# Kernel tuning notes

Hardware: AMD Instinct MI355X
Metric: run time of the kernel (lower is better)

The kernel has to match this reference:

```python
import jax, jax.numpy as jnp
import numpy as np

B, N, D = 2, 8192, 1024
H, DH = 8, 64  # heads, dim_head; inner = H*DH = 512
INNER = H * DH


def setup_inputs() -> dict:
    key = jax.random.key(0)
    k1, k2, k3 = jax.random.split(key, 3)
    x = jax.random.normal(k1, (B, N, D), dtype=jnp.float32)
    # xavier_uniform-ish scaling for weights
    W_qkv = jax.random.normal(k2, (D, 3 * INNER), dtype=jnp.float32) * (1.0 / np.sqrt(D))
    W_out = jax.random.normal(k3, (INNER, D), dtype=jnp.float32) * (1.0 / np.sqrt(INNER))
    b_out = jnp.zeros((D,), dtype=jnp.float32)
    return {"x": x, "W_qkv": W_qkv, "W_out": W_out, "b_out": b_out}


def reference(x, W_qkv, W_out, b_out):
    b, n, d = x.shape
    qkv = x @ W_qkv                               # [b, n, 3*inner]
    q, k, v = jnp.split(qkv, 3, axis=-1)          # each [b, n, inner]

    def to_heads(t):
        return t.reshape(b, n, H, DH).transpose(0, 2, 1, 3)  # [b, h, n, dh]

    q, k, v = to_heads(q), to_heads(k), to_heads(v)
    q = jax.nn.softmax(q, axis=-1)                # over dim_head
    k = jax.nn.softmax(k, axis=-2)                # over sequence
    # context: k^T v  -> [b, h, dh, dh]
    context = jnp.einsum('bhnd,bhne->bhde', k, v)
    out = jnp.einsum('bhnd,bhde->bhne', q, context)  # [b, h, n, dh]
    out = out.transpose(0, 2, 1, 3).reshape(b, n, INNER)
    return out @ W_out + b_out                    # [b, n, d]
```

## Files before the change

kernel.cpp:

```cpp
#include <hip/hip_runtime.h>
#include <stdint.h>


typedef _Float16 half4 __attribute__((ext_vector_type(4)));
typedef _Float16 half8 __attribute__((ext_vector_type(8)));
typedef float f32x4 __attribute__((ext_vector_type(4)));

#define WS_XB 0UL
#define WS_WQKVT 33554432UL
#define WS_CWT 37748736UL
#define WS_EKH 54525952UL
#define WS_VH 71303168UL
#define WS_SQ 88080384UL
#define WS_CTXPART 104857600UL
#define WS_COLPART 113246208UL
#define WS_CTX 113377280UL

__device__ __forceinline__ void gld16(const void* g, void* l) {
  __builtin_amdgcn_global_load_lds(
      (const __attribute__((address_space(1))) unsigned int*)g,
      (__attribute__((address_space(3))) unsigned int*)l, 16, 0, 0);
}

__global__ void prep_kernel(const float* __restrict__ x,
                            const float* __restrict__ Wqkv,
                            _Float16* __restrict__ xb,
                            _Float16* __restrict__ wqkvT) {
  const int blk = blockIdx.x;
  if (blk < 16384) {
    int i = blk * 256 + threadIdx.x;
    f32x4 v = *(const f32x4*)(x + (size_t)i * 4);
    half4 h = {(_Float16)v[0], (_Float16)v[1], (_Float16)v[2], (_Float16)v[3]};
    *(half4*)(xb + (size_t)i * 4) = h;
  } else {
    int i = (blk - 16384) * 256 + threadIdx.x;
    int c = i >> 10, r = i & 1023;
    wqkvT[i] = (_Float16)Wqkv[(size_t)r * 1536 + c];
  }
}


__device__ __forceinline__ void stage_tile(const _Float16* __restrict__ G, int K,
                                           int rowbase, int kt, char* region,
                                           int t) {
  char* wbase = region + (t & ~63) * 16;
#pragma unroll
  for (int q = 0; q < 4; ++q) {
    const int row = q * 32 + (t >> 3);
    const int col8 = ((t & 7) ^ (row & 7)) * 8;
    gld16(G + (size_t)(rowbase + row) * K + kt + col8, wbase + q * 4096);
  }
}

template <int EPI>
__global__ __launch_bounds__(256, 2) void gemm128(
    const _Float16* __restrict__ A, const _Float16* __restrict__ BT, int K,
    int NTN, int bstride, _Float16* __restrict__ oQ, _Float16* __restrict__ oK,
    _Float16* __restrict__ oV, float* __restrict__ oC,
    const float* __restrict__ bias) {
  __shared__ char lds[65536];
  const int t = threadIdx.x;
  const int l = t & 63, w = t >> 6;
  const int wm = w >> 1, wn = w & 1;
  const int fr = l & 15, qq = l >> 4;
  const int swzx = (fr & 7) << 4;

  const int nwg = gridDim.x;
  const int cpx = nwg >> 3;
  const int wg = (blockIdx.x & 7) * cpx + (blockIdx.x >> 3);
  const int tileM = wg / NTN, tileN = wg - tileM * NTN;
  const int mbase = tileM * 128, nbase = tileN * 128;
  BT += (size_t)(tileM >> 6) * bstride;

  const int NT = K >> 6;
  f32x4 acc[4][4] = {};
  half8 a[4][2], b[4][2];

  auto STG = [&](int tile) {
    int kt = tile * 64;
    if (kt > K - 64) kt = K - 64;
    char* base = lds + ((tile & 1) << 15);
    stage_tile(A, K, mbase, kt, base, t);
    stage_tile(BT, K, nbase, kt, base + 16384, t);
  };

  STG(0);
  STG(1);
  asm volatile("s_waitcnt vmcnt(8)" ::: "memory");
  __builtin_amdgcn_s_barrier();

  for (int t2 = 0; t2 < NT; ++t2) {
    const char* ldsA = lds + ((t2 & 1) << 15);
    const char* ldsB = ldsA + 16384;
    STG(t2 + 1);
#pragma unroll
    for (int mi = 0; mi < 4; ++mi)
#pragma unroll
      for (int kk = 0; kk < 2; ++kk) {
        int off = (wm * 64 + mi * 16 + fr) * 128 + ((kk * 64 + qq * 16) ^ swzx);
        a[mi][kk] = *(const half8*)(ldsA + off);
      }
#pragma unroll
    for (int ni = 0; ni < 4; ++ni)
#pragma unroll
      for (int kk = 0; kk < 2; ++kk) {
        int off = (wn * 64 + ni * 16 + fr) * 128 + ((kk * 64 + qq * 16) ^ swzx);
        b[ni][kk] = *(const half8*)(ldsB + off);
      }
    __builtin_amdgcn_s_barrier();
    __builtin_amdgcn_s_setprio(1);
#pragma unroll
    for (int mi = 0; mi < 4; ++mi)
#pragma unroll
      for (int ni = 0; ni < 2; ++ni)
#pragma unroll
        for (int kk = 0; kk < 2; ++kk)
          acc[mi][ni] = __builtin_amdgcn_mfma_f32_16x16x32_f16(
              a[mi][kk], b[ni][kk], acc[mi][ni], 0, 0, 0);
    __builtin_amdgcn_s_setprio(0);
    asm volatile("s_waitcnt vmcnt(0) lgkmcnt(0)" ::: "memory");
    __builtin_amdgcn_s_barrier();
    __builtin_amdgcn_s_setprio(1);
#pragma unroll
    for (int mi = 0; mi < 4; ++mi)
#pragma unroll
      for (int ni = 2; ni < 4; ++ni)
#pragma unroll
        for (int kk = 0; kk < 2; ++kk)
          acc[mi][ni] = __builtin_amdgcn_mfma_f32_16x16x32_f16(
              a[mi][kk], b[ni][kk], acc[mi][ni], 0, 0, 0);
    __builtin_amdgcn_s_setprio(0);
  }

  if (EPI == 0) {
    const int gcol0 = nbase + wn * 64;
    const int which = gcol0 >> 9;
    if (which == 0) {
#pragma unroll
      for (int mi = 0; mi < 4; ++mi) {
        const int grow = mbase + wm * 64 + mi * 16 + qq * 4;
        float e[4][4], rs[4];
#pragma unroll
        for (int r = 0; r < 4; ++r) {
          float s = 0.f;
#pragma unroll
          for (int ni = 0; ni < 4; ++ni) {
            e[ni][r] = __expf(acc[mi][ni][r]);
            s += e[ni][r];
          }
#pragma unroll
          for (int off = 1; off < 16; off <<= 1) s += __shfl_xor(s, off, 64);
          rs[r] = 1.f / s;
        }
#pragma unroll
        for (int ni = 0; ni < 4; ++ni) {
          const int gcol = gcol0 + ni * 16 + fr;
#pragma unroll
          for (int r = 0; r < 4; ++r)
            oQ[(size_t)(grow + r) * 512 + gcol] = (_Float16)(e[ni][r] * rs[r]);
        }
      }
    } else {
      _Float16* dst0 = (which == 1) ? oK : oV;
      const int h = (gcol0 >> 6) & 7;
#pragma unroll
      for (int mi = 0; mi < 4; ++mi) {
        const int grow = mbase + wm * 64 + mi * 16 + qq * 4;
        const int bidx = grow >> 13, n = grow & 8191;
        const size_t rb = ((size_t)((bidx << 3) + h) * 8192 + n) * 64;
#pragma unroll
        for (int ni = 0; ni < 4; ++ni) {
          const int d = ni * 16 + fr;
#pragma unroll
          for (int r = 0; r < 4; ++r) {
            float v = acc[mi][ni][r];
            if (which == 1) v = __expf(v);
            dst0[rb + (size_t)r * 64 + d] = (_Float16)v;
          }
        }
      }
    }
  } else {
#pragma unroll
    for (int mi = 0; mi < 4; ++mi) {
      const int grow = mbase + wm * 64 + mi * 16 + qq * 4;
#pragma unroll
      for (int ni = 0; ni < 4; ++ni) {
        const int gcol = nbase + wn * 64 + ni * 16 + fr;
        const float bb = bias[gcol];
#pragma unroll
        for (int r = 0; r < 4; ++r)
          oC[(size_t)(grow + r) * 1024 + gcol] = acc[mi][ni][r] + bb;
      }
    }
  }
}

__global__ __launch_bounds__(256) void ctx_partial_kernel(
    const _Float16* __restrict__ ekh, const _Float16* __restrict__ vh,
    float* __restrict__ ctxpart, float* __restrict__ colpart) {
  __shared__ float se[128 * 64];
  __shared__ float sv[128 * 64];
  const int t = threadIdx.x;
  const int bh = blockIdx.x >> 5, ch = blockIdx.x & 31;
  const size_t rowbase = ((size_t)bh * 8192 + ch * 256) * 64;
  const int d0 = (t & 15) * 4, e0 = (t >> 4) * 4;
  float acc[4][4] = {};
  float colacc = 0.f;
  for (int sub = 0; sub < 2; ++sub) {
    const _Float16* kp = ekh + rowbase + (size_t)sub * (128 * 64);
    const _Float16* vp = vh + rowbase + (size_t)sub * (128 * 64);
    __syncthreads();
    for (int i = t; i < 2048; i += 256) {
      half4 a = ((const half4*)kp)[i];
      half4 b = ((const half4*)vp)[i];
      f32x4 fa = {(float)a[0], (float)a[1], (float)a[2], (float)a[3]};
      f32x4 fb = {(float)b[0], (float)b[1], (float)b[2], (float)b[3]};
      *(f32x4*)&se[i * 4] = fa;
      *(f32x4*)&sv[i * 4] = fb;
    }
    __syncthreads();
    if (t < 64) {
      for (int n = 0; n < 128; ++n) colacc += se[n * 64 + t];
    }
    for (int n = 0; n < 128; ++n) {
      f32x4 a = *(const f32x4*)&se[n * 64 + d0];
      f32x4 b = *(const f32x4*)&sv[n * 64 + e0];
#pragma unroll
      for (int i2 = 0; i2 < 4; ++i2)
#pragma unroll
        for (int j = 0; j < 4; ++j) acc[i2][j] += a[i2] * b[j];
    }
  }
  float* cp = ctxpart + (size_t)blockIdx.x * 4096;
#pragma unroll
  for (int i2 = 0; i2 < 4; ++i2)
#pragma unroll
    for (int j = 0; j < 4; ++j) cp[(d0 + i2) * 64 + e0 + j] = acc[i2][j];
  if (t < 64) colpart[blockIdx.x * 64 + t] = colacc;
}

__global__ void ctx_reduce_kernel(const float* __restrict__ ctxpart,
                                  const float* __restrict__ colpart,
                                  float* __restrict__ ctx) {
  int i = blockIdx.x * 256 + threadIdx.x;
  int bh = i >> 12, r = i & 4095, d = r >> 6;
  float s = 0.f, v = 0.f;
  for (int c = 0; c < 32; ++c) {
    s += colpart[((size_t)bh * 32 + c) * 64 + d];
    v += ctxpart[((size_t)bh * 32 + c) * 4096 + r];
  }
  ctx[i] = v / s;
}

__global__ __launch_bounds__(256) void ctxw_kernel(const float* __restrict__ ctx,
                                                   const float* __restrict__ Wout,
                                                   _Float16* __restrict__ cwT) {
  const int blk = blockIdx.x;
  const int bh = blk >> 6, d = blk & 63;
  const int b = bh >> 3, h = bh & 7;
  const int t = threadIdx.x;
  const float* crow = ctx + (size_t)bh * 4096 + d * 64;
  float acc[4] = {};
#pragma unroll 8
  for (int e = 0; e < 64; ++e) {
    const float c = crow[e];
    const float* wr = Wout + (size_t)(h * 64 + e) * 1024 + t;
#pragma unroll
    for (int j = 0; j < 4; ++j) acc[j] += c * wr[j * 256];
  }
  _Float16* dst = cwT + (size_t)b * 524288 + (size_t)t * 512 + h * 64 + d;
#pragma unroll
  for (int j = 0; j < 4; ++j) dst[(size_t)j * 256 * 512] = (_Float16)acc[j];
}

extern "C" void kernel_launch(void* const* d_in, const int* in_sizes, int n_in,
                              void* d_out, int out_size, void* d_ws, size_t ws_size,
                              hipStream_t stream) {
  const float* x = (const float*)d_in[0];
  const float* Wqkv = (const float*)d_in[1];
  const float* Wout = (const float*)d_in[2];
  const float* bout = (const float*)d_in[3];
  float* out = (float*)d_out;
  char* ws = (char*)d_ws;

  _Float16* xb = (_Float16*)(ws + WS_XB);
  _Float16* wqkvT = (_Float16*)(ws + WS_WQKVT);
  _Float16* cwT = (_Float16*)(ws + WS_CWT);
  _Float16* ekh = (_Float16*)(ws + WS_EKH);
  _Float16* vh = (_Float16*)(ws + WS_VH);
  _Float16* sq = (_Float16*)(ws + WS_SQ);
  float* ctxpart = (float*)(ws + WS_CTXPART);
  float* colpart = (float*)(ws + WS_COLPART);
  float* ctx = (float*)(ws + WS_CTX);

  prep_kernel<<<22528, 256, 0, stream>>>(x, Wqkv, xb, wqkvT);
  gemm128<0><<<1536, 256, 0, stream>>>(xb, wqkvT, 1024, 12, 0, sq, ekh, vh,
                                       nullptr, nullptr);
  ctx_partial_kernel<<<512, 256, 0, stream>>>(ekh, vh, ctxpart, colpart);
  ctx_reduce_kernel<<<256, 256, 0, stream>>>(ctxpart, colpart, ctx);
  ctxw_kernel<<<1024, 256, 0, stream>>>(ctx, Wout, cwT);
  gemm128<1><<<1024, 256, 0, stream>>>(sq, cwT, 512, 8, 524288, nullptr,
                                       nullptr, nullptr, out, bout);
}
```

Baseline: 157.3 us.

## Fuse context reduction into ctxw and rework ctx_partial with async LDS loads

The context partial kernel now loads the fp16 k/v tiles straight into LDS with global_load_lds instead of converting them to fp32 in shared memory. Each wave handles 64 rows with an 8x8 per-lane outer product, and the four waves' partials are reduced through LDS. The separate ctx_reduce kernel is removed: ctxw now sums the 32 chunk partials and the column sums itself before multiplying by W_out. This saves a launch and a global round-trip, but each ctxw block redoes reduction work that is shared across blocks, and the 64KB LDS footprint limits occupancy.

```diff
diff --git a/kernel.cpp b/kernel.cpp
--- a/kernel.cpp
+++ b/kernel.cpp
@@ -14,7 +14,6 @@
 #define WS_SQ 88080384UL
 #define WS_CTXPART 104857600UL
 #define WS_COLPART 113246208UL
-#define WS_CTX 113377280UL
 
 __device__ __forceinline__ void gld16(const void* g, void* l) {
   __builtin_amdgcn_global_load_lds(
@@ -196,76 +195,107 @@
   }
 }
 
-__global__ __launch_bounds__(256) void ctx_partial_kernel(
+__global__ __launch_bounds__(256, 2) void ctx_partial_kernel(
     const _Float16* __restrict__ ekh, const _Float16* __restrict__ vh,
     float* __restrict__ ctxpart, float* __restrict__ colpart) {
-  __shared__ float se[128 * 64];
-  __shared__ float sv[128 * 64];
-  const int t = threadIdx.x;
+  __shared__ char smem[65536];
+  __shared__ float credu[4][64];
+  _Float16* sek = (_Float16*)smem;
+  _Float16* svv = (_Float16*)(smem + 32768);
+  const int t = threadIdx.x, l = t & 63, w = t >> 6;
   const int bh = blockIdx.x >> 5, ch = blockIdx.x & 31;
   const size_t rowbase = ((size_t)bh * 8192 + ch * 256) * 64;
-  const int d0 = (t & 15) * 4, e0 = (t >> 4) * 4;
-  float acc[4][4] = {};
-  float colacc = 0.f;
-  for (int sub = 0; sub < 2; ++sub) {
-    const _Float16* kp = ekh + rowbase + (size_t)sub * (128 * 64);
-    const _Float16* vp = vh + rowbase + (size_t)sub * (128 * 64);
-    __syncthreads();
-    for (int i = t; i < 2048; i += 256) {
-      half4 a = ((const half4*)kp)[i];
-      half4 b = ((const half4*)vp)[i];
-      f32x4 fa = {(float)a[0], (float)a[1], (float)a[2], (float)a[3]};
-      f32x4 fb = {(float)b[0], (float)b[1], (float)b[2], (float)b[3]};
-      *(f32x4*)&se[i * 4] = fa;
-      *(f32x4*)&sv[i * 4] = fb;
+  {
+    const char* eksrc = (const char*)(ekh + rowbase);
+    const char* vsrc = (const char*)(vh + rowbase);
+    char* ekbase = smem + w * 1024;
+    char* vbase = smem + 32768 + w * 1024;
+#pragma unroll
+    for (int s = 0; s < 8; ++s) {
+      gld16(eksrc + (size_t)(s * 256 + t) * 16, ekbase + s * 4096);
+      gld16(vsrc + (size_t)(s * 256 + t) * 16, vbase + s * 4096);
     }
-    __syncthreads();
-    if (t < 64) {
-      for (int n = 0; n < 128; ++n) colacc += se[n * 64 + t];
+  }
+  asm volatile("s_waitcnt vmcnt(0)" ::: "memory");
+  __builtin_amdgcn_s_barrier();
+
+  const int d0 = (l & 7) * 8, e0 = (l >> 3) * 8;
+  f32x4 acc[8][2] = {};
+  float cacc[8] = {};
+  const int n0 = w * 64;
+  for (int n = n0; n < n0 + 64; ++n) {
+    half8 k8 = *(const half8*)&sek[n * 64 + d0];
+    half8 v8 = *(const half8*)&svv[n * 64 + e0];
+    float e[8];
+    f32x4 v4[2];
+#pragma unroll
+    for (int i = 0; i < 8; ++i) e[i] = (float)k8[i];
+#pragma unroll
+    for (int j = 0; j < 8; ++j) v4[j >> 2][j & 3] = (float)v8[j];
+#pragma unroll
+    for (int i = 0; i < 8; ++i) {
+      cacc[i] += e[i];
+      acc[i][0] += v4[0] * e[i];
+      acc[i][1] += v4[1] * e[i];
     }
-    for (int n = 0; n < 128; ++n) {
-      f32x4 a = *(const f32x4*)&se[n * 64 + d0];
-      f32x4 b = *(const f32x4*)&sv[n * 64 + e0];
-#pragma unroll
-      for (int i2 = 0; i2 < 4; ++i2)
-#pragma unroll
-        for (int j = 0; j < 4; ++j) acc[i2][j] += a[i2] * b[j];
-    }
-  }
+  }
+  __builtin_amdgcn_s_barrier();
+  float* red = (float*)smem;
+#pragma unroll
+  for (int i = 0; i < 8; ++i) {
+    *(f32x4*)&red[w * 4096 + (d0 + i) * 64 + e0] = acc[i][0];
+    *(f32x4*)&red[w * 4096 + (d0 + i) * 64 + e0 + 4] = acc[i][1];
+  }
+  if (l < 8) {
+#pragma unroll
+    for (int i = 0; i < 8; ++i) credu[w][l * 8 + i] = cacc[i];
+  }
+  __syncthreads();
   float* cp = ctxpart + (size_t)blockIdx.x * 4096;
 #pragma unroll
-  for (int i2 = 0; i2 < 4; ++i2)
-#pragma unroll
-    for (int j = 0; j < 4; ++j) cp[(d0 + i2) * 64 + e0 + j] = acc[i2][j];
-  if (t < 64) colpart[blockIdx.x * 64 + t] = colacc;
-}
-
-__global__ void ctx_reduce_kernel(const float* __restrict__ ctxpart,
-                                  const float* __restrict__ colpart,
-                                  float* __restrict__ ctx) {
-  int i = blockIdx.x * 256 + threadIdx.x;
-  int bh = i >> 12, r = i & 4095, d = r >> 6;
-  float s = 0.f, v = 0.f;
-  for (int c = 0; c < 32; ++c) {
-    s += colpart[((size_t)bh * 32 + c) * 64 + d];
-    v += ctxpart[((size_t)bh * 32 + c) * 4096 + r];
-  }
-  ctx[i] = v / s;
-}
-
-__global__ __launch_bounds__(256) void ctxw_kernel(const float* __restrict__ ctx,
-                                                   const float* __restrict__ Wout,
-                                                   _Float16* __restrict__ cwT) {
+  for (int s = 0; s < 4; ++s) {
+    const int r = t * 16 + s * 4;
+    f32x4 sum = *(const f32x4*)&red[r];
+    sum += *(const f32x4*)&red[4096 + r];
+    sum += *(const f32x4*)&red[8192 + r];
+    sum += *(const f32x4*)&red[12288 + r];
+    *(f32x4*)&cp[r] = sum;
+  }
+  if (t < 64)
+    colpart[blockIdx.x * 64 + t] =
+        credu[0][t] + credu[1][t] + credu[2][t] + credu[3][t];
+}
+
+__global__ __launch_bounds__(256) void ctxw_kernel(
+    const float* __restrict__ ctxpart, const float* __restrict__ colpart,
+    const float* __restrict__ Wout, _Float16* __restrict__ cwT) {
+  __shared__ float part[4][64];
+  __shared__ float csp[32];
+  __shared__ float crow[64];
   const int blk = blockIdx.x;
   const int bh = blk >> 6, d = blk & 63;
   const int b = bh >> 3, h = bh & 7;
   const int t = threadIdx.x;
-  const float* crow = ctx + (size_t)bh * 4096 + d * 64;
+  const int e = t & 63, cq = t >> 6;
+  float p = 0.f;
+#pragma unroll
+  for (int cc = 0; cc < 8; ++cc)
+    p += ctxpart[(size_t)(bh * 32 + cq * 8 + cc) * 4096 + d * 64 + e];
+  part[cq][e] = p;
+  if (t >= 64 && t < 96)
+    csp[t - 64] = colpart[(size_t)(bh * 32 + (t - 64)) * 64 + d];
+  __syncthreads();
+  if (t < 64) {
+    float csum = 0.f;
+#pragma unroll
+    for (int c = 0; c < 32; ++c) csum += csp[c];
+    crow[t] = (part[0][t] + part[1][t] + part[2][t] + part[3][t]) / csum;
+  }
+  __syncthreads();
   float acc[4] = {};
-#pragma unroll 8
-  for (int e = 0; e < 64; ++e) {
-    const float c = crow[e];
-    const float* wr = Wout + (size_t)(h * 64 + e) * 1024 + t;
+  for (int e2 = 0; e2 < 64; ++e2) {
+    const float c = crow[e2];
+    const float* wr = Wout + (size_t)(h * 64 + e2) * 1024 + t;
 #pragma unroll
     for (int j = 0; j < 4; ++j) acc[j] += c * wr[j * 256];
   }
@@ -292,14 +322,12 @@
   _Float16* sq = (_Float16*)(ws + WS_SQ);
   float* ctxpart = (float*)(ws + WS_CTXPART);
   float* colpart = (float*)(ws + WS_COLPART);
-  float* ctx = (float*)(ws + WS_CTX);
 
   prep_kernel<<<22528, 256, 0, stream>>>(x, Wqkv, xb, wqkvT);
   gemm128<0><<<1536, 256, 0, stream>>>(xb, wqkvT, 1024, 12, 0, sq, ekh, vh,
                                        nullptr, nullptr);
   ctx_partial_kernel<<<512, 256, 0, stream>>>(ekh, vh, ctxpart, colpart);
-  ctx_reduce_kernel<<<256, 256, 0, stream>>>(ctxpart, colpart, ctx);
-  ctxw_kernel<<<1024, 256, 0, stream>>>(ctx, Wout, cwT);
+  ctxw_kernel<<<1024, 256, 0, stream>>>(ctxpart, colpart, Wout, cwT);
   gemm128<1><<<1024, 256, 0, stream>>>(sq, cwT, 512, 8, 524288, nullptr,
                                        nullptr, nullptr, out, bout);
 }
```

Measured after the change: 162.6 us. +3.3%, slower.
